# Kernel tuning notes

Hardware: AMD Instinct MI355X
Metric: run time of the kernel (lower is better)

The kernel has to match this reference:

```python
import jax, jax.numpy as jnp
import numpy as np

F_DIM = 256  # hidden_features == input_features
O_DIM = 256  # out_features
N_NODES = 13
B = 16384


def _edge_index():
    # edge_index1/2/3 from GraphNet.create_edge_index, then append reversed edges
    src = np.array([0, 0, 0, 0, 1, 2, 3, 4, 5, 6, 7, 8], dtype=np.int32)
    dst = np.array([1, 2, 3, 4, 5, 6, 7, 8, 9, 10, 11, 12], dtype=np.int32)
    src_all = np.concatenate([src, dst])
    dst_all = np.concatenate([dst, src])
    return jnp.asarray(src_all), jnp.asarray(dst_all)


def setup_inputs() -> dict:
    key = jax.random.key(0)
    ks = jax.random.split(key, 16)
    def lin(k, fan_in, fan_out):
        kw, kb = jax.random.split(k)
        s = 1.0 / np.sqrt(fan_in)
        return (jax.random.uniform(kw, (fan_in, fan_out), jnp.float32, -s, s),
                jax.random.uniform(kb, (fan_out,), jnp.float32, -s, s))
    x = jax.random.normal(ks[0], (B, 64), jnp.float32)
    w_in1, b_in1 = lin(ks[1], 16, F_DIM)
    w_in2, b_in2 = lin(ks[2], 4, F_DIM)
    w1_1, b1_1 = lin(ks[3], 2 * F_DIM, F_DIM)
    w2_1, b2_1 = lin(ks[4], F_DIM, F_DIM)
    w1_2, b1_2 = lin(ks[5], 2 * F_DIM, F_DIM)
    w2_2, b2_2 = lin(ks[6], F_DIM, F_DIM)
    w1_3, b1_3 = lin(ks[7], 2 * F_DIM, F_DIM)
    w2_3, b2_3 = lin(ks[8], F_DIM, O_DIM)
    edge_src, edge_dst = _edge_index()
    return dict(x=x, edge_src=edge_src, edge_dst=edge_dst,
                w_in1=w_in1, b_in1=b_in1, w_in2=w_in2, b_in2=b_in2,
                w1_1=w1_1, b1_1=b1_1, w2_1=w2_1, b2_1=b2_1,
                w1_2=w1_2, b1_2=b1_2, w2_2=w2_2, b2_2=b2_2,
                w1_3=w1_3, b1_3=b1_3, w2_3=w2_3, b2_3=b2_3)


def _create_features(x):
    object_feature = x[:, :16]  # [B,16]
    # joint k -> column offset j: k<4 -> k ; 4<=k<8 -> 2(k-4)+4 ; 8<=k<12 -> 2(k-8)+5
    js = jnp.array([0, 1, 2, 3, 4, 6, 8, 10, 5, 7, 9, 11], dtype=jnp.int32)
    offs = jnp.array([0, 12, 24, 36], dtype=jnp.int32)
    idx = 16 + js[:, None] + offs[None, :]  # [12,4]
    joint_feature = x[:, idx]  # [B,12,4]
    return object_feature, joint_feature


def _graph_layer(h, src, dst, w1, b1, w2, b2):
    # gather: h_j = source nodes, h_i = target nodes
    h_i = h[:, dst]  # [B,E,F]
    h_j = h[:, src]  # [B,E,F]
    m = jnp.concatenate([h_i, h_j], axis=-1)  # [B,E,2F]
    m = jax.nn.elu(m @ w1 + b1)
    m = jax.nn.elu(m @ w2 + b2)  # [B,E,O]
    # scatter-max over target index; every node has >=1 incoming edge so no -inf survives
    out = jnp.full((h.shape[0], N_NODES, m.shape[-1]), -jnp.inf, m.dtype)
    out = out.at[:, dst].max(m)
    return out


def reference(x, edge_src, edge_dst, w_in1, b_in1, w_in2, b_in2,
              w1_1, b1_1, w2_1, b2_1, w1_2, b1_2, w2_2, b2_2,
              w1_3, b1_3, w2_3, b2_3):
    obj, joint = _create_features(x)
    obj_in = obj @ w_in1 + b_in1                      # [B,F]
    joint_in = joint @ w_in2 + b_in2                  # [B,12,F]
    h = jnp.concatenate([obj_in[:, None, :], joint_in], axis=1)  # [B,13,F]
    h = _graph_layer(h, edge_src, edge_dst, w1_1, b1_1, w2_1, b2_1)
    h = _graph_layer(h, edge_src, edge_dst, w1_2, b1_2, w2_2, b2_2)
    h = _graph_layer(h, edge_src, edge_dst, w1_3, b1_3, w2_3, b2_3)
    return h
```

## Files before the change

### kernel.cpp

```cpp
#include <hip/hip_runtime.h>
#include <hip/hip_bf16.h>

typedef unsigned short ushort_t;
typedef __attribute__((ext_vector_type(4))) short bf16x4;
typedef __attribute__((ext_vector_type(8))) short bf16x8;
typedef __attribute__((ext_vector_type(16))) float floatx16;

#define BT 4
#define HSTR 264
#define M1STR 264
#define HELEMS (52*HSTR)
#define M1ELEMS (96*M1STR)

__constant__ int SRCT[24] = {0,0,0,0,1,2,3,4,5,6,7,8, 1,2,3,4,5,6,7,8,9,10,11,12};
__constant__ int DSTT[24] = {1,2,3,4,5,6,7,8,9,10,11,12, 0,0,0,0,1,2,3,4,5,6,7,8};
__constant__ int JS[12]   = {0,1,2,3,4,6,8,10,5,7,9,11};

__device__ inline float b2f(ushort_t u) {
  __hip_bfloat16 b = *reinterpret_cast<__hip_bfloat16*>(&u);
  return __bfloat162float(b);
}
__device__ inline ushort_t f2b(float f) {
  __hip_bfloat16 b = __float2bfloat16(f);
  return *reinterpret_cast<ushort_t*>(&b);
}
__device__ inline float ldv(const void* p, size_t i, int isf) {
  return isf ? ((const float*)p)[i] : b2f(((const ushort_t*)p)[i]);
}
__device__ inline float eluf(float v) { return v > 0.f ? v : (__expf(v) - 1.f); }

#define CELL(r) (a2[(r)>>5][((r)&3) + 4*(((r)>>3)&3)])

__global__ void detect_dtype(const ushort_t* __restrict__ x, int* __restrict__ flag) {
  int t = threadIdx.x;
  int cnt = 0;
  for (int i = t; i < 512; i += 64) {
    int e = (x[i] >> 7) & 0xFF;
    cnt += (e >= 160) ? 1 : 0;
  }
  #pragma unroll
  for (int o = 32; o > 0; o >>= 1) cnt += __shfl_down(cnt, o);
  if (t == 0) *flag = (cnt >= 8) ? 1 : 0;
}

__global__ void repack_weights(
    const void* __restrict__ w1_0, const void* __restrict__ w1_1, const void* __restrict__ w1_2,
    const void* __restrict__ w2_0, const void* __restrict__ w2_1, const void* __restrict__ w2_2,
    ushort_t* __restrict__ W1R, ushort_t* __restrict__ W2R,
    const int* __restrict__ flag)
{
  const int isf = *flag;
  int b = blockIdx.x;
  int lane = threadIdx.x;
  int h = lane >> 5, li = lane & 31;
  if (b < 768) {
    int l = b >> 8, rem = b & 255;
    int kk = rem & 31;
    int ntg = rem >> 5;
    const void* w1 = (l == 0) ? w1_0 : (l == 1 ? w1_1 : w1_2);
    int k0 = kk*16 + h*8;
    int n  = ntg*32 + li;
    ushort_t* dst = W1R + (((size_t)l*256 + rem)*64 + lane)*8;
    #pragma unroll
    for (int j = 0; j < 8; ++j) dst[j] = f2b(ldv(w1, (size_t)(k0+j)*256 + n, isf));
  } else {
    int bb = b - 768;
    int l = bb >> 7, rem = bb & 127;
    int kk = rem & 15;
    int nt = rem >> 4;
    const void* w2 = (l == 0) ? w2_0 : (l == 1 ? w2_1 : w2_2);
    int k0 = kk*16 + h*8;
    int n  = nt*32 + li;
    ushort_t* dst = W2R + (((size_t)l*128 + rem)*64 + lane)*8;
    #pragma unroll
    for (int j = 0; j < 8; ++j) dst[j] = f2b(ldv(w2, (size_t)(k0+j)*256 + n, isf));
  }
}

__global__ __launch_bounds__(512, 4) void graphnet_main(
    const void* __restrict__ x,
    const void* __restrict__ w_in1, const void* __restrict__ b_in1,
    const void* __restrict__ w_in2, const void* __restrict__ b_in2,
    const void* __restrict__ b1a, const void* __restrict__ b1b, const void* __restrict__ b1c,
    const void* __restrict__ b2a, const void* __restrict__ b2b, const void* __restrict__ b2c,
    const ushort_t* __restrict__ W1R, const ushort_t* __restrict__ W2R,
    void* __restrict__ outp, const int* __restrict__ flag)
{
  __shared__ __align__(16) ushort_t Hbuf[HELEMS];
  __shared__ __align__(16) ushort_t m1buf[M1ELEMS];

  const int isf  = *flag;
  const int tid  = threadIdx.x;
  const int w    = tid >> 6;
  const int lane = tid & 63;
  const int li   = lane & 31;
  const int h    = lane >> 5;
  const int b0   = blockIdx.x * BT;

  if (tid < 256) {
    int bb = tid >> 6, cc = tid & 63;
    m1buf[tid] = f2b(ldv(x, (size_t)(b0 + bb)*64 + cc, isf));
  }
  __syncthreads();
  {
    const int c  = tid & 255;
    const int bh = tid >> 8;
    float wf[16], wj[4];
    #pragma unroll
    for (int k = 0; k < 16; ++k) wf[k] = ldv(w_in1, k*256 + c, isf);
    #pragma unroll
    for (int o = 0; o < 4; ++o)  wj[o] = ldv(w_in2, o*256 + c, isf);
    float bo = ldv(b_in1, c, isf);
    float bj = ldv(b_in2, c, isf);
    #pragma unroll
    for (int bi = 0; bi < 2; ++bi) {
      int bb = bh*2 + bi;
      float s = bo;
      #pragma unroll
      for (int k = 0; k < 16; ++k) s += b2f(m1buf[bb*64 + k]) * wf[k];
      Hbuf[(bb*13 + 0)*HSTR + c] = f2b(s);
      #pragma unroll
      for (int jj = 0; jj < 12; ++jj) {
        float t = bj;
        #pragma unroll
        for (int o = 0; o < 4; ++o)
          t += b2f(m1buf[bb*64 + 16 + JS[jj] + 12*o]) * wj[o];
        Hbuf[(bb*13 + 1 + jj)*HSTR + c] = f2b(t);
      }
    }
  }
  __syncthreads();

  int offD[3], offS[3];
  #pragma unroll
  for (int mt = 0; mt < 3; ++mt) {
    int er = 32*mt + li;
    int bb = er / 24;
    int e  = er - 24*bb;
    offD[mt] = (bb*13 + DSTT[e]) * HSTR;
    offS[mt] = (bb*13 + SRCT[e]) * HSTR;
  }

  for (int l = 0; l < 3; ++l) {
    const void* b1p  = (l == 0) ? b1a : (l == 1 ? b1b : b1c);
    const void* b2p  = (l == 0) ? b2a : (l == 1 ? b2b : b2c);
    const ushort_t* W1Rl = W1R + (size_t)l*131072;
    const ushort_t* W2Rl = W2R + (size_t)l*65536;

    floatx16 a1[3];
    #pragma unroll
    for (int mt = 0; mt < 3; ++mt)
      #pragma unroll
      for (int r = 0; r < 16; ++r) a1[mt][r] = 0.f;

    const ushort_t* wp = W1Rl + ((size_t)w*32*64 + lane)*8;
    #pragma unroll
    for (int ro = 0; ro < 2; ++ro) {
      #pragma unroll 8
      for (int kq = 0; kq < 16; ++kq) {
        int kk = ro*16 + kq;
        bf16x8 wfr = *reinterpret_cast<const bf16x8*>(wp + kk*512);
        int kb = kq*16 + h*8;
        #pragma unroll
        for (int mt = 0; mt < 3; ++mt) {
          int ao = (ro ? offS[mt] : offD[mt]) + kb;
          bf16x8 hfr = *reinterpret_cast<const bf16x8*>(&Hbuf[ao]);
          a1[mt] = __builtin_amdgcn_mfma_f32_32x32x16_bf16(wfr, hfr, a1[mt], 0, 0, 0);
        }
      }
    }

    {
      float b1s[16];
      #pragma unroll
      for (int r = 0; r < 16; ++r)
        b1s[r] = ldv(b1p, w*32 + (r&3) + 8*(r>>2) + 4*h, isf);
      #pragma unroll
      for (int mt = 0; mt < 3; ++mt) {
        #pragma unroll
        for (int g = 0; g < 4; ++g) {
          bf16x4 pk;
          #pragma unroll
          for (int d = 0; d < 4; ++d)
            pk[d] = (short)f2b(eluf(a1[mt][4*g + d] + b1s[4*g + d]));
          *reinterpret_cast<bf16x4*>(&m1buf[(32*mt + li)*M1STR + w*32 + 8*g + 4*h]) = pk;
        }
      }
    }
    __syncthreads();

    floatx16 a2[3];
    #pragma unroll
    for (int mt = 0; mt < 3; ++mt)
      #pragma unroll
      for (int r = 0; r < 16; ++r) a2[mt][r] = 0.f;

    #pragma unroll 8
    for (int kk = 0; kk < 16; ++kk) {
      bf16x8 bfr = *reinterpret_cast<const bf16x8*>(W2Rl + (((size_t)w*16 + kk)*64 + lane)*8);
      #pragma unroll
      for (int mt = 0; mt < 3; ++mt) {
        bf16x8 afr = *reinterpret_cast<const bf16x8*>(&m1buf[(32*mt + li)*M1STR + kk*16 + h*8]);
        a2[mt] = __builtin_amdgcn_mfma_f32_32x32x16_bf16(afr, bfr, a2[mt], 0, 0, 0);
      }
    }

    {
      const int c = w*32 + li;
      float b2v = ldv(b2p, c, isf);
      auto emit = [&](int bb, int node, float v) {
        float vf = eluf(v + b2v);
        if (l == 2) {
          size_t o = ((size_t)(b0 + bb)*13 + node)*256 + c;
          if (isf) ((float*)outp)[o] = vf;
          else     ((ushort_t*)outp)[o] = f2b(vf);
        } else {
          Hbuf[(bb*13 + node)*HSTR + c] = f2b(vf);
        }
      };
      #pragma unroll
      for (int bb = 0; bb < BT; ++bb) {
        #pragma unroll
        for (int j = 0; j < 4; ++j) {
          int rA = 24*bb + j;
          float vA = fmaxf(CELL(rA), CELL(rA + 16));
          emit(bb, 1 + j + 4*h, vA);
        }
        float c0v = CELL(24*bb + 8);
        float c1v = CELL(24*bb + 9);
        float c2v = CELL(24*bb + 10);
        float c3v = CELL(24*bb + 11);
        if (h == 0) {
          emit(bb, 9,  c0v); emit(bb, 10, c1v);
          emit(bb, 11, c2v); emit(bb, 12, c3v);
        } else {
          emit(bb, 0, fmaxf(fmaxf(c0v, c1v), fmaxf(c2v, c3v)));
        }
      }
    }
    __syncthreads();
  }
}

extern "C" void kernel_launch(void* const* d_in, const int* in_sizes, int n_in,
                              void* d_out, int out_size, void* d_ws, size_t ws_size,
                              hipStream_t stream) {
  const void* x     = d_in[0];
  const void* w_in1 = d_in[3];
  const void* b_in1 = d_in[4];
  const void* w_in2 = d_in[5];
  const void* b_in2 = d_in[6];
  const void* w1_1  = d_in[7];
  const void* b1_1  = d_in[8];
  const void* w2_1  = d_in[9];
  const void* b2_1  = d_in[10];
  const void* w1_2  = d_in[11];
  const void* b1_2  = d_in[12];
  const void* w2_2  = d_in[13];
  const void* b2_2  = d_in[14];
  const void* w1_3  = d_in[15];
  const void* b1_3  = d_in[16];
  const void* w2_3  = d_in[17];
  const void* b2_3  = d_in[18];

  int* flag     = (int*)d_ws;
  ushort_t* W1R = (ushort_t*)((char*)d_ws + 64);
  ushort_t* W2R = W1R + 3*131072;

  detect_dtype<<<1, 64, 0, stream>>>((const ushort_t*)x, flag);
  repack_weights<<<1152, 64, 0, stream>>>(w1_1, w1_2, w1_3, w2_1, w2_2, w2_3, W1R, W2R, flag);

  graphnet_main<<<16384 / BT, 512, 0, stream>>>(
      x, w_in1, b_in1, w_in2, b_in2,
      b1_1, b1_2, b1_3, b2_1, b2_2, b2_3,
      W1R, W2R, d_out, flag);
}
```

Before: 966.6 us.

## Process edge tiles sequentially to shrink m1 buffer and raise occupancy

The layer loop now handles one 32-row edge tile at a time instead of all three at once. For each tile it runs the first GEMM, applies ELU, writes to a single-tile m1 buffer and runs the second GEMM. This cuts LDS use for m1 to a third and needs only one first-layer accumulator, which lets the kernel request 6 blocks per CU instead of 4. In exchange, weight fragments are reloaded from global memory for every tile, losing the old reuse across three tiles. Each tile also adds two block-wide barriers.

```diff
diff --git a/kernel.cpp b/kernel.cpp
--- a/kernel.cpp
+++ b/kernel.cpp
@@ -10,7 +10,7 @@
 #define HSTR 264
 #define M1STR 264
 #define HELEMS (52*HSTR)
-#define M1ELEMS (96*M1STR)
+#define M1ELEMS (32*M1STR)
 
 __constant__ int SRCT[24] = {0,0,0,0,1,2,3,4,5,6,7,8, 1,2,3,4,5,6,7,8,9,10,11,12};
 __constant__ int DSTT[24] = {1,2,3,4,5,6,7,8,9,10,11,12, 0,0,0,0,1,2,3,4,5,6,7,8};
@@ -77,7 +77,7 @@
   }
 }
 
-__global__ __launch_bounds__(512, 4) void graphnet_main(
+__global__ __launch_bounds__(512, 6) void graphnet_main(
     const void* __restrict__ x,
     const void* __restrict__ w_in1, const void* __restrict__ b_in1,
     const void* __restrict__ w_in2, const void* __restrict__ b_in2,
@@ -147,60 +147,50 @@
     const ushort_t* W1Rl = W1R + (size_t)l*131072;
     const ushort_t* W2Rl = W2R + (size_t)l*65536;
 
-    floatx16 a1[3];
-    #pragma unroll
-    for (int mt = 0; mt < 3; ++mt)
-      #pragma unroll
-      for (int r = 0; r < 16; ++r) a1[mt][r] = 0.f;
-
-    const ushort_t* wp = W1Rl + ((size_t)w*32*64 + lane)*8;
-    #pragma unroll
-    for (int ro = 0; ro < 2; ++ro) {
-      #pragma unroll 8
-      for (int kq = 0; kq < 16; ++kq) {
-        int kk = ro*16 + kq;
-        bf16x8 wfr = *reinterpret_cast<const bf16x8*>(wp + kk*512);
-        int kb = kq*16 + h*8;
-        #pragma unroll
-        for (int mt = 0; mt < 3; ++mt) {
-          int ao = (ro ? offS[mt] : offD[mt]) + kb;
-          bf16x8 hfr = *reinterpret_cast<const bf16x8*>(&Hbuf[ao]);
-          a1[mt] = __builtin_amdgcn_mfma_f32_32x32x16_bf16(wfr, hfr, a1[mt], 0, 0, 0);
-        }
-      }
-    }
-
-    {
+    floatx16 a2[3];
+
+    #pragma unroll
+    for (int mt = 0; mt < 3; ++mt) {
+      floatx16 a1;
+      #pragma unroll
+      for (int r = 0; r < 16; ++r) a1[r] = 0.f;
+
+      const ushort_t* wp = W1Rl + ((size_t)w*32*64 + lane)*8;
+      #pragma unroll
+      for (int ro = 0; ro < 2; ++ro) {
+        const int ob = ro ? offS[mt] : offD[mt];
+        #pragma unroll 4
+        for (int kq = 0; kq < 16; ++kq) {
+          int kk = ro*16 + kq;
+          bf16x8 wfr = *reinterpret_cast<const bf16x8*>(wp + kk*512);
+          bf16x8 hfr = *reinterpret_cast<const bf16x8*>(&Hbuf[ob + kq*16 + h*8]);
+          a1 = __builtin_amdgcn_mfma_f32_32x32x16_bf16(wfr, hfr, a1, 0, 0, 0);
+        }
+      }
+
       float b1s[16];
       #pragma unroll
       for (int r = 0; r < 16; ++r)
         b1s[r] = ldv(b1p, w*32 + (r&3) + 8*(r>>2) + 4*h, isf);
-      #pragma unroll
-      for (int mt = 0; mt < 3; ++mt) {
+
+      __syncthreads();
+
+      #pragma unroll
+      for (int g = 0; g < 4; ++g) {
+        bf16x4 pk;
         #pragma unroll
-        for (int g = 0; g < 4; ++g) {
-          bf16x4 pk;
-          #pragma unroll
-          for (int d = 0; d < 4; ++d)
-            pk[d] = (short)f2b(eluf(a1[mt][4*g + d] + b1s[4*g + d]));
-          *reinterpret_cast<bf16x4*>(&m1buf[(32*mt + li)*M1STR + w*32 + 8*g + 4*h]) = pk;
-        }
-      }
-    }
-    __syncthreads();
-
-    floatx16 a2[3];
-    #pragma unroll
-    for (int mt = 0; mt < 3; ++mt)
+        for (int d = 0; d < 4; ++d)
+          pk[d] = (short)f2b(eluf(a1[4*g + d] + b1s[4*g + d]));
+        *reinterpret_cast<bf16x4*>(&m1buf[li*M1STR + w*32 + 8*g + 4*h]) = pk;
+      }
+      __syncthreads();
+
       #pragma unroll
       for (int r = 0; r < 16; ++r) a2[mt][r] = 0.f;
-
-    #pragma unroll 8
-    for (int kk = 0; kk < 16; ++kk) {
-      bf16x8 bfr = *reinterpret_cast<const bf16x8*>(W2Rl + (((size_t)w*16 + kk)*64 + lane)*8);
-      #pragma unroll
-      for (int mt = 0; mt < 3; ++mt) {
-        bf16x8 afr = *reinterpret_cast<const bf16x8*>(&m1buf[(32*mt + li)*M1STR + kk*16 + h*8]);
+      #pragma unroll 4
+      for (int kk = 0; kk < 16; ++kk) {
+        bf16x8 bfr = *reinterpret_cast<const bf16x8*>(W2Rl + (((size_t)w*16 + kk)*64 + lane)*8);
+        bf16x8 afr = *reinterpret_cast<const bf16x8*>(&m1buf[li*M1STR + kk*16 + h*8]);
         a2[mt] = __builtin_amdgcn_mfma_f32_32x32x16_bf16(afr, bfr, a2[mt], 0, 0, 0);
       }
     }
```

Result: slower. 1.503 ms (+55.5%).
